# Kernel optimization log

Hardware: AMD Instinct MI355X
Metric: run time of the kernel (lower is better)

Reference implementation:

```python
import jax, jax.numpy as jnp
import numpy as np

R, N, B, S = 20, 4096, 16, 256          # relations, total nodes, graphs, nodes per graph
DIN, HID, H = 512, 128, 4               # in_dim, hidden_dim, num_heads
D = HID * H                              # flattened node-feature width (=512)
E = 16384                                # edges per relation
NEG_SLOPE = 0.2


def _gat(h, src, dst, W, al, ar, b):
    # DGL GATConv, eval mode (dropout off), identity residual (in == H*out), allow_zero_in_degree
    z = (h @ W).reshape(N, H, HID)                        # [N,H,Dh]
    el = (z * al).sum(-1)                                 # [N,H]
    er = (z * ar).sum(-1)                                 # [N,H]
    e = jax.nn.leaky_relu(el[src] + er[dst], NEG_SLOPE)   # [E,H]
    m = jax.ops.segment_max(e, dst, num_segments=N)       # per-dst max (edge softmax)
    ex = jnp.exp(e - m[dst])
    den = jax.ops.segment_sum(ex, dst, num_segments=N)
    alpha = ex / den[dst]                                 # [E,H]
    agg = jax.ops.segment_sum(alpha[..., None] * z[src], dst, num_segments=N)
    return agg + h.reshape(N, H, HID) + b, alpha


def _rgat_conv(h, src, dst, W, al, ar, b):
    # HeteroGraphConv with aggregate='mean' over R relations; scan keeps memory flat
    def body(acc, xs):
        s, d, Wr, alr, arr, br = xs
        out, alpha = _gat(h, s, d, Wr, alr, arr, br)
        return acc + out, alpha.mean(-1)                  # attention meaned over heads -> [E]
    acc, attn = jax.lax.scan(body, jnp.zeros((N, H, HID), h.dtype), (src, dst, W, al, ar, b))
    return acc / R, attn                                  # [N,H,Dh], [R,E]


def setup_inputs() -> dict:
    key = jax.random.key(0)
    ks = jax.random.split(key, 24)
    f32 = jnp.float32
    p = lambda k, shape: jax.random.normal(k, shape, f32) * 0.05
    z = lambda shape: jnp.zeros(shape, f32)
    return {
        'feat': jax.random.normal(ks[0], (N, DIN), f32),
        'hyp_emb': jax.random.normal(ks[1], (B, D), f32),
        'edge_src': jax.random.randint(ks[2], (R, E), 0, N),
        'edge_dst': jax.random.randint(ks[3], (R, E), 0, N),
        'W1': p(ks[4], (R, DIN, H * HID)), 'al1': p(ks[5], (R, H, HID)), 'ar1': p(ks[6], (R, H, HID)), 'b1': z((R, H, HID)),
        'W2': p(ks[7], (R, D, H * HID)), 'al2': p(ks[8], (R, H, HID)), 'ar2': p(ks[9], (R, H, HID)), 'b2': z((R, H, HID)),
        'Wq': p(ks[10], (D, D)), 'bq': z(D), 'Wk': p(ks[11], (D, D)), 'bk': z(D),
        'Wv': p(ks[12], (D, D)), 'bv': z(D), 'Wo': p(ks[13], (D, D)), 'bo': z(D),
        'Wn1': p(ks[14], (2 * D, HID)), 'bn1': z(HID), 'Wn2': p(ks[15], (HID, 2)), 'bn2': z(2),
    }


def reference(feat, hyp_emb, edge_src, edge_dst,
              W1, al1, ar1, b1, W2, al2, ar2, b2,
              Wq, bq, Wk, bk, Wv, bv, Wo, bo, Wn1, bn1, Wn2, bn2):
    # --- RGAT (rgat_generation) layer 1 + attention weights ---
    h1, attn = _rgat_conv(feat, edge_src, edge_dst, W1, al1, ar1, b1)
    h1 = jax.nn.elu(h1.reshape(N, D))
    # --- layer 2 ---
    h2, _ = _rgat_conv(h1, edge_src, edge_dst, W2, al2, ar2, b2)
    feats = h2.reshape(N, D)
    # --- node importance: scatter-add edge attention onto dst nodes, summed over etypes ---
    imp = jax.ops.segment_sum(attn.reshape(-1), edge_dst.reshape(-1), num_segments=N)
    feats_p = feats.reshape(B, S, D)                      # uniform graphs: split+pad == reshape
    weighted = feats_p * imp.reshape(B, S)[..., None]
    # --- MultiheadAttention(embed=D, heads=4): query = hyp_emb broadcast to all S positions ---
    Hm, Dm = 4, D // 4
    q = (hyp_emb @ Wq + bq).reshape(B, Hm, 1, Dm)         # identical query at every position
    k = (feats_p @ Wk + bk).reshape(B, S, Hm, Dm).transpose(0, 2, 1, 3)
    v = (feats_p @ Wv + bv).reshape(B, S, Hm, Dm).transpose(0, 2, 1, 3)
    scores = jnp.einsum('bhqd,bhkd->bhqk', q, k) / jnp.sqrt(jnp.float32(Dm))
    a = jax.nn.softmax(scores, axis=-1)                   # [B,Hm,1,S]
    ctx = jnp.einsum('bhqk,bhkd->bhqd', a, v).reshape(B, 1, D)
    attn_out = jnp.broadcast_to(ctx @ Wo + bo, (B, S, D))
    # --- node classifier on concat(weighted feats, attention output) ---
    combined = jnp.concatenate([weighted, attn_out], axis=-1).reshape(N, 2 * D)
    node_logits = jax.nn.relu(combined @ Wn1 + bn1) @ Wn2 + bn2
    return node_logits, attn
```

## Files before the change

### kernel.cpp

```cpp
#include <hip/hip_runtime.h>
#include <hip/hip_bf16.h>
#include <math.h>

#define NREL 20
#define NN   4096
#define NE   16384
#define DF   512
#define NHD  4
#define DHH  128
#define NB   16
#define NS   256

typedef __attribute__((ext_vector_type(8))) __bf16 bf16x8;
typedef __attribute__((ext_vector_type(4))) float f32x4;

__device__ inline float bf2f(unsigned short u) {
    union { float f; unsigned int i; } c; c.i = ((unsigned int)u) << 16; return c.f;
}
__device__ inline unsigned short f2bu(float f) {
    union { __hip_bfloat16 b; unsigned short u; } c; c.b = __float2bfloat16(f); return c.u;
}
__device__ inline void storeOut(float* p, float v) { *p = v; }
__device__ inline void storeOut(__hip_bfloat16* p, float v) { *p = __float2bfloat16(v); }

__device__ inline void load_lds16(const __hip_bfloat16* g, __hip_bfloat16* l) {
    __builtin_amdgcn_global_load_lds(
        (const __attribute__((address_space(1))) unsigned int*)(const void*)g,
        (__attribute__((address_space(3))) unsigned int*)(void*)l, 16, 0, 0);
}

__global__ void count_kernel(const int* __restrict__ dst, int* __restrict__ cnt) {
    int idx = blockIdx.x * 256 + threadIdx.x;
    int r = idx / NE;
    atomicAdd(&cnt[r * NN + dst[idx]], 1);
}

__global__ void sumcnt_kernel(const int* __restrict__ cnt, int* __restrict__ cntAll) {
    int n = blockIdx.x * 256 + threadIdx.x;
    int s = 0;
    #pragma unroll
    for (int r = 0; r < NREL; ++r) s += cnt[r * NN + n];
    cntAll[n] = s;
}

__global__ void scan_kernel(const int* __restrict__ cnt, int* __restrict__ rowptr,
                            int* __restrict__ woff) {
    int r = blockIdx.x;
    int t = threadIdx.x;
    __shared__ int sums[1024];
    int v[4]; int local = 0;
    #pragma unroll
    for (int j = 0; j < 4; ++j) { v[j] = cnt[r * NN + t * 4 + j]; local += v[j]; }
    sums[t] = local;
    __syncthreads();
    for (int off = 1; off < 1024; off <<= 1) {
        int x = (t >= off) ? sums[t - off] : 0;
        __syncthreads();
        sums[t] += x;
        __syncthreads();
    }
    int run = (t == 0) ? 0 : sums[t - 1];
    #pragma unroll
    for (int j = 0; j < 4; ++j) {
        rowptr[r * (NN + 1) + t * 4 + j] = run;
        woff[r * NN + t * 4 + j] = run;
        run += v[j];
    }
    if (t == 1023) rowptr[r * (NN + 1) + NN] = run;
}

__global__ void fill_kernel(const int* __restrict__ dst, const int* __restrict__ src,
                            int* __restrict__ woff, int* __restrict__ srcCSR,
                            int* __restrict__ eidCSR) {
    int idx = blockIdx.x * 256 + threadIdx.x;
    int r = idx / NE; int e = idx % NE;
    int pos = atomicAdd(&woff[r * NN + dst[idx]], 1);
    srcCSR[r * NE + pos] = src[idx];
    eidCSR[r * NE + pos] = e;
}

__global__ void cast_kernel(const float* __restrict__ in, unsigned short* __restrict__ out) {
    int i = blockIdx.x * 256 + threadIdx.x;
    float4 v = ((const float4*)in)[i];
    ushort4 o;
    o.x = f2bu(v.x); o.y = f2bu(v.y); o.z = f2bu(v.z); o.w = f2bu(v.w);
    ((ushort4*)out)[i] = o;
}

__global__ void biassum_kernel(const float* __restrict__ bmat, float* __restrict__ bsum) {
    int f = blockIdx.x * 256 + threadIdx.x;
    float s = 0.f;
    #pragma unroll
    for (int r = 0; r < NREL; ++r) s += bmat[r * DF + f];
    bsum[f] = s;
}

__global__ __launch_bounds__(256) void transw_kernel(
    const float* __restrict__ W, __hip_bfloat16* __restrict__ Wt, int K, int N)
{
    int r = blockIdx.z;
    __shared__ float t[32][33];
    int k0 = blockIdx.x * 32, n0 = blockIdx.y * 32;
    int tx = threadIdx.x % 32, ty = threadIdx.x / 32;
    #pragma unroll
    for (int kk = ty; kk < 32; kk += 8)
        t[kk][tx] = W[((size_t)r * K + k0 + kk) * N + n0 + tx];
    __syncthreads();
    #pragma unroll
    for (int nn = ty; nn < 32; nn += 8)
        Wt[((size_t)r * N + n0 + nn) * K + k0 + tx] = __float2bfloat16(t[tx][nn]);
}

template <typename OutT, bool RELU, bool FUSE>
__global__ __launch_bounds__(256) void mfma_gemm(
    const __hip_bfloat16* __restrict__ A,
    const __hip_bfloat16* __restrict__ BtAll,
    const float* __restrict__ bias,
    OutT* __restrict__ Call, int M, int N, int K,
    const float* __restrict__ al, const float* __restrict__ ar,
    float* __restrict__ el, float* __restrict__ er)
{
    int r = blockIdx.z;
    const __hip_bfloat16* Bt = BtAll + (size_t)r * N * K;
    OutT* C = Call + (size_t)r * M * N;
    const int rowBase = blockIdx.y * 128;
    const int colBase = blockIdx.x * 128;
    __shared__ __hip_bfloat16 As[128 * 32];
    __shared__ __hip_bfloat16 Bs[128 * 32];
    const int tid = threadIdx.x;
    const int w = tid >> 6, l = tid & 63;
    const int wr = w >> 1, wc = w & 1;
    const int m15 = l & 15, q = l >> 4;
    const int sRow = w * 16 + (l >> 2);
    const int sKs = (((l & 3) ^ ((l >> 3) & 3))) * 8;
    const __hip_bfloat16* Ag0 = A + (size_t)(rowBase + sRow) * K + sKs;
    const __hip_bfloat16* Ag1 = Ag0 + (size_t)64 * K;
    const __hip_bfloat16* Bg0 = Bt + (size_t)(colBase + sRow) * K + sKs;
    const __hip_bfloat16* Bg1 = Bg0 + (size_t)64 * K;
    __hip_bfloat16* Asl0 = As + sRow * 32 + (l & 3) * 8;
    __hip_bfloat16* Asl1 = Asl0 + 2048;
    __hip_bfloat16* Bsl0 = Bs + sRow * 32 + (l & 3) * 8;
    __hip_bfloat16* Bsl1 = Bsl0 + 2048;
    const int swf = (m15 >> 1) & 3;

    f32x4 acc[4][4];
    #pragma unroll
    for (int i = 0; i < 4; ++i)
        #pragma unroll
        for (int j = 0; j < 4; ++j) acc[i][j] = (f32x4){0.f, 0.f, 0.f, 0.f};

    for (int k0 = 0; k0 < K; k0 += 32) {
        load_lds16(Ag0 + k0, Asl0);
        load_lds16(Ag1 + k0, Asl1);
        load_lds16(Bg0 + k0, Bsl0);
        load_lds16(Bg1 + k0, Bsl1);
        __syncthreads();
        bf16x8 a[4], b[4];
        #pragma unroll
        for (int i = 0; i < 4; ++i)
            a[i] = *(const bf16x8*)&As[(wr * 64 + i * 16 + m15) * 32 + (q ^ swf) * 8];
        #pragma unroll
        for (int j = 0; j < 4; ++j)
            b[j] = *(const bf16x8*)&Bs[(wc * 64 + j * 16 + m15) * 32 + (q ^ swf) * 8];
        #pragma unroll
        for (int i = 0; i < 4; ++i)
            #pragma unroll
            for (int j = 0; j < 4; ++j)
                acc[i][j] = __builtin_amdgcn_mfma_f32_16x16x32_bf16(a[i], b[j], acc[i][j], 0, 0, 0);
        __syncthreads();
    }

    #pragma unroll
    for (int i = 0; i < 4; ++i) {
        #pragma unroll
        for (int j = 0; j < 4; ++j) {
            int col = colBase + wc * 64 + j * 16 + m15;
            float bv = bias ? bias[col] : 0.f;
            #pragma unroll
            for (int reg = 0; reg < 4; ++reg) {
                int row = rowBase + wr * 64 + i * 16 + q * 4 + reg;
                float v = acc[i][j][reg] + bv;
                if (RELU) v = fmaxf(v, 0.f);
                storeOut(&C[(size_t)row * N + col], v);
            }
        }
    }

    if (FUSE) {
        float alv[4], arv[4];
        #pragma unroll
        for (int j = 0; j < 4; ++j) {
            int col = colBase + wc * 64 + j * 16 + m15;
            alv[j] = al[r * DF + col];
            arv[j] = ar[r * DF + col];
        }
        float pe[4][4], pr[4][4];
        #pragma unroll
        for (int i = 0; i < 4; ++i)
            #pragma unroll
            for (int reg = 0; reg < 4; ++reg) {
                float se = 0.f, sr = 0.f;
                #pragma unroll
                for (int j = 0; j < 4; ++j) {
                    se += acc[i][j][reg] * alv[j];
                    sr += acc[i][j][reg] * arv[j];
                }
                pe[i][reg] = se; pr[i][reg] = sr;
            }
        #pragma unroll
        for (int off = 1; off < 16; off <<= 1)
            #pragma unroll
            for (int i = 0; i < 4; ++i)
                #pragma unroll
                for (int reg = 0; reg < 4; ++reg) {
                    pe[i][reg] += __shfl_xor(pe[i][reg], off);
                    pr[i][reg] += __shfl_xor(pr[i][reg], off);
                }
        float* eP = (float*)As;
        float* rP = eP + 256;
        if (m15 == 0) {
            #pragma unroll
            for (int i = 0; i < 4; ++i)
                #pragma unroll
                for (int reg = 0; reg < 4; ++reg) {
                    int rowL = wr * 64 + i * 16 + q * 4 + reg;
                    eP[rowL * 2 + wc] = pe[i][reg];
                    rP[rowL * 2 + wc] = pr[i][reg];
                }
        }
        __syncthreads();
        if (tid < 128) {
            int head = colBase >> 7;
            size_t idx = ((size_t)r * NN + rowBase + tid) * NHD + head;
            el[idx] = eP[tid * 2] + eP[tid * 2 + 1];
            er[idx] = rP[tid * 2] + rP[tid * 2 + 1];
        }
    }
}

template <typename OutT>
__global__ __launch_bounds__(256) void gemm_kernel(
    const float* __restrict__ A, const float* __restrict__ Bm,
    const float* __restrict__ bias, OutT* __restrict__ C,
    int M, int K, int Nn)
{
    int r = blockIdx.z;
    const float* B = Bm + (size_t)r * K * Nn;
    OutT* Cr = C + (size_t)r * M * Nn;
    int rowBase = blockIdx.y * 64;
    int colBase = blockIdx.x * 64;
    __shared__ float As[64][17];
    __shared__ float Bs[16][64];
    int tid = threadIdx.x;
    int tx = tid % 16, ty = tid / 16;
    float acc[4][4] = {};
    int aRow = tid / 4, aK4 = (tid % 4) * 4;
    int bK = tid / 16, bN4 = (tid % 16) * 4;
    for (int k0 = 0; k0 < K; k0 += 16) {
        int gRow = rowBase + aRow;
        float4 av = make_float4(0.f, 0.f, 0.f, 0.f);
        if (gRow < M) av = *(const float4*)(A + (size_t)gRow * K + k0 + aK4);
        As[aRow][aK4 + 0] = av.x; As[aRow][aK4 + 1] = av.y;
        As[aRow][aK4 + 2] = av.z; As[aRow][aK4 + 3] = av.w;
        float4 bv = *(const float4*)(B + (size_t)(k0 + bK) * Nn + colBase + bN4);
        *(float4*)&Bs[bK][bN4] = bv;
        __syncthreads();
        #pragma unroll
        for (int k = 0; k < 16; ++k) {
            float a[4], b[4];
            #pragma unroll
            for (int i = 0; i < 4; ++i) a[i] = As[ty * 4 + i][k];
            #pragma unroll
            for (int j = 0; j < 4; ++j) b[j] = Bs[k][tx * 4 + j];
            #pragma unroll
            for (int i = 0; i < 4; ++i)
                #pragma unroll
                for (int j = 0; j < 4; ++j) acc[i][j] += a[i] * b[j];
        }
        __syncthreads();
    }
    #pragma unroll
    for (int i = 0; i < 4; ++i) {
        int gRow = rowBase + ty * 4 + i;
        if (gRow >= M) continue;
        #pragma unroll
        for (int j = 0; j < 4; ++j) {
            int gCol = colBase + tx * 4 + j;
            float v = acc[i][j];
            if (bias) v += bias[gCol];
            storeOut(&Cr[(size_t)gRow * Nn + gCol], v);
        }
    }
}

__global__ __launch_bounds__(256) void alpha_kernel(
    const float* __restrict__ el, const float* __restrict__ er,
    const int* __restrict__ rowptr, const int* __restrict__ rowptr2,
    const int* __restrict__ cnt, const int* __restrict__ srcCSR,
    const int* __restrict__ eidCSR,
    float* __restrict__ alphaPk, int* __restrict__ srcPk,
    float* __restrict__ attn, float* __restrict__ imp)
{
    int t = blockIdx.x * 256 + threadIdx.x;
    int r = t / NN, n = t % NN;
    int start = rowptr[r * (NN + 1) + n];
    int d = rowptr[r * (NN + 1) + n + 1] - start;
    if (d == 0) return;
    float4 er4 = *(const float4*)&er[((size_t)r * NN + n) * NHD];
    float4 den = make_float4(0.f, 0.f, 0.f, 0.f);
    for (int j = 0; j < d; ++j) {
        int s = srcCSR[r * NE + start + j];
        float4 el4 = *(const float4*)&el[((size_t)r * NN + s) * NHD];
        float v0 = el4.x + er4.x; v0 = v0 > 0.f ? v0 : 0.2f * v0;
        float v1 = el4.y + er4.y; v1 = v1 > 0.f ? v1 : 0.2f * v1;
        float v2 = el4.z + er4.z; v2 = v2 > 0.f ? v2 : 0.2f * v2;
        float v3 = el4.w + er4.w; v3 = v3 > 0.f ? v3 : 0.2f * v3;
        den.x += __expf(v0); den.y += __expf(v1);
        den.z += __expf(v2); den.w += __expf(v3);
    }
    float4 inv = make_float4(1.f / den.x, 1.f / den.y, 1.f / den.z, 1.f / den.w);
    int pbase = rowptr2[n];
    for (int rp = 0; rp < r; ++rp) pbase += cnt[rp * NN + n];
    float impLoc = 0.f;
    for (int j = 0; j < d; ++j) {
        int s = srcCSR[r * NE + start + j];
        float4 el4 = *(const float4*)&el[((size_t)r * NN + s) * NHD];
        float v0 = el4.x + er4.x; v0 = v0 > 0.f ? v0 : 0.2f * v0;
        float v1 = el4.y + er4.y; v1 = v1 > 0.f ? v1 : 0.2f * v1;
        float v2 = el4.z + er4.z; v2 = v2 > 0.f ? v2 : 0.2f * v2;
        float v3 = el4.w + er4.w; v3 = v3 > 0.f ? v3 : 0.2f * v3;
        float4 a4 = make_float4(__expf(v0) * inv.x, __expf(v1) * inv.y,
                                __expf(v2) * inv.z, __expf(v3) * inv.w);
        *(float4*)&alphaPk[(size_t)(pbase + j) * 4] = a4;
        srcPk[pbase + j] = r * NN + s;
        if (attn) {
            float a = 0.25f * (a4.x + a4.y + a4.z + a4.w);
            attn[r * NE + eidCSR[r * NE + start + j]] = a;
            impLoc += a;
        }
    }
    if (attn) atomicAdd(&imp[n], impLoc);
}

__global__ __launch_bounds__(256) void aggc_kernel(
    const __hip_bfloat16* __restrict__ Z,
    const int* __restrict__ rowptr2, const int* __restrict__ srcPk,
    const float* __restrict__ alphaPk, const float* __restrict__ bsum,
    const float* __restrict__ hin, float* __restrict__ hout,
    __hip_bfloat16* __restrict__ hout_bf, int applyElu)
{
    int n = blockIdx.x;
    int w = threadIdx.x >> 6, lane = threadIdx.x & 63;
    int h = lane >> 4;
    int base = rowptr2[n];
    int deg = rowptr2[n + 1] - base;
    float acc[8] = {};
    int i = w * 2;
    int z0 = 0, z1 = 0; float a0 = 0.f, a1 = 0.f;
    if (i < deg)     { z0 = srcPk[base + i];     a0 = alphaPk[(size_t)(base + i) * 4 + h]; }
    if (i + 1 < deg) { z1 = srcPk[base + i + 1]; a1 = alphaPk[(size_t)(base + i + 1) * 4 + h]; }
    while (i < deg) {
        int cz0 = z0, cz1 = z1; float ca0 = a0, ca1 = a1;
        int ni = i + 8;
        if (ni < deg)     { z0 = srcPk[base + ni];     a0 = alphaPk[(size_t)(base + ni) * 4 + h]; }
        if (ni + 1 < deg) { z1 = srcPk[base + ni + 1]; a1 = alphaPk[(size_t)(base + ni + 1) * 4 + h]; }
        else a1 = 0.f;
        float4 r0 = *(const float4*)&Z[(size_t)cz0 * DF + lane * 8];
        float4 r1 = *(const float4*)&Z[(size_t)cz1 * DF + lane * 8];
        const unsigned short* u0 = (const unsigned short*)&r0;
        const unsigned short* u1 = (const unsigned short*)&r1;
        #pragma unroll
        for (int j = 0; j < 8; ++j) acc[j] += ca0 * bf2f(u0[j]) + ca1 * bf2f(u1[j]);
        i = ni;
    }
    __shared__ float red[4][DF];
    #pragma unroll
    for (int j = 0; j < 8; ++j) red[w][lane * 8 + j] = acc[j];
    __syncthreads();
    const float invR = 1.0f / NREL;
    int f = threadIdx.x;
    #pragma unroll
    for (int rep = 0; rep < 2; ++rep, f += 256) {
        float v = red[0][f] + red[1][f] + red[2][f] + red[3][f];
        v = (v + bsum[f]) * invR + hin[(size_t)n * DF + f];
        if (applyElu) v = v > 0.f ? v : expm1f(v);
        hout[(size_t)n * DF + f] = v;
        hout_bf[(size_t)n * DF + f] = __float2bfloat16(v);
    }
}

__global__ __launch_bounds__(256) void mha_scores(
    const float* __restrict__ q, const float* __restrict__ k,
    float* __restrict__ scores)
{
    int b = blockIdx.x;
    int w = threadIdx.x >> 6, lane = threadIdx.x & 63;
    int s = blockIdx.y * 4 + w;
    const float4* qp = (const float4*)&q[(size_t)b * DF + lane * 8];
    const float4* kp = (const float4*)&k[((size_t)(b * NS + s)) * DF + lane * 8];
    float4 q0 = qp[0], q1 = qp[1];
    float4 k0 = kp[0], k1 = kp[1];
    float p = q0.x * k0.x + q0.y * k0.y + q0.z * k0.z + q0.w * k0.w
            + q1.x * k1.x + q1.y * k1.y + q1.z * k1.z + q1.w * k1.w;
    #pragma unroll
    for (int off = 1; off < 16; off <<= 1) p += __shfl_xor(p, off);
    if ((lane & 15) == 0) {
        int h = lane >> 4;
        scores[((size_t)(b * NHD + h)) * NS + s] = p * 0.08838834764831845f;
    }
}

__global__ __launch_bounds__(256) void mha_soft(float* __restrict__ scores) {
    int b = blockIdx.x;
    int h = threadIdx.x >> 6, lane = threadIdx.x & 63;
    float* sp = &scores[((size_t)(b * NHD + h)) * NS];
    float v[4];
    float mx = -INFINITY;
    #pragma unroll
    for (int i = 0; i < 4; ++i) { v[i] = sp[lane + 64 * i]; mx = fmaxf(mx, v[i]); }
    #pragma unroll
    for (int off = 32; off; off >>= 1) mx = fmaxf(mx, __shfl_xor(mx, off));
    float sum = 0.f;
    #pragma unroll
    for (int i = 0; i < 4; ++i) { v[i] = __expf(v[i] - mx); sum += v[i]; }
    #pragma unroll
    for (int off = 32; off; off >>= 1) sum += __shfl_xor(sum, off);
    float inv = 1.0f / sum;
    #pragma unroll
    for (int i = 0; i < 4; ++i) sp[lane + 64 * i] = v[i] * inv;
}

__global__ __launch_bounds__(256) void mha_ctx(
    const float* __restrict__ scores, const float* __restrict__ v,
    float* __restrict__ ctx)
{
    int b = blockIdx.x, h = blockIdx.y;
    int t = threadIdx.x;
    int d = t & 127, half = t >> 7;
    __shared__ float a_s[NS];
    a_s[t] = scores[((size_t)(b * NHD + h)) * NS + t];
    __syncthreads();
    float acc = 0.f;
    const float* vp = &v[((size_t)(b * NS + half * 128)) * DF + h * DHH + d];
    #pragma unroll 4
    for (int i = 0; i < 128; ++i)
        acc += a_s[half * 128 + i] * vp[(size_t)i * DF];
    __shared__ float red[256];
    red[t] = acc;
    __syncthreads();
    if (t < 128) ctx[(size_t)b * DF + h * DHH + t] = red[t] + red[t + 128];
}

__global__ __launch_bounds__(256) void combined_kernel(
    const float* __restrict__ feats, const float* __restrict__ imp,
    const float* __restrict__ abuf, __hip_bfloat16* __restrict__ comb)
{
    int n = blockIdx.x;
    int t = threadIdx.x;
    int b = n >> 8;
    float im = imp[n];
    #pragma unroll
    for (int rep = 0; rep < 4; ++rep) {
        int f = t + rep * 256;
        float v = (f < DF) ? feats[(size_t)n * DF + f] * im
                           : abuf[(size_t)b * DF + (f - DF)];
        comb[(size_t)n * (2 * DF) + f] = __float2bfloat16(v);
    }
}

__global__ __launch_bounds__(256) void cls2_kernel(
    const float* __restrict__ hidden, const float* __restrict__ Wn2,
    const float* __restrict__ bn2, float* __restrict__ out)
{
    __shared__ float w2[256];
    int t = threadIdx.x;
    w2[t] = Wn2[t];
    __syncthreads();
    int n = blockIdx.x * 256 + t;
    const float* hp = &hidden[(size_t)n * 128];
    float p0 = bn2[0], p1 = bn2[1];
    #pragma unroll 4
    for (int kk = 0; kk < 128; ++kk) {
        float hv = hp[kk];
        p0 += hv * w2[kk * 2 + 0];
        p1 += hv * w2[kk * 2 + 1];
    }
    out[n * 2 + 0] = p0;
    out[n * 2 + 1] = p1;
}

extern "C" void kernel_launch(void* const* d_in, const int* in_sizes, int n_in,
                              void* d_out, int out_size, void* d_ws, size_t ws_size,
                              hipStream_t stream) {
    const float* feat = (const float*)d_in[0];
    const float* hyp  = (const float*)d_in[1];
    const int*   esrc = (const int*)d_in[2];
    const int*   edst = (const int*)d_in[3];
    const float* W1   = (const float*)d_in[4];
    const float* al1  = (const float*)d_in[5];
    const float* ar1  = (const float*)d_in[6];
    const float* b1   = (const float*)d_in[7];
    const float* W2   = (const float*)d_in[8];
    const float* al2  = (const float*)d_in[9];
    const float* ar2  = (const float*)d_in[10];
    const float* b2   = (const float*)d_in[11];
    const float* Wq = (const float*)d_in[12]; const float* bq = (const float*)d_in[13];
    const float* Wk = (const float*)d_in[14]; const float* bk = (const float*)d_in[15];
    const float* Wv = (const float*)d_in[16]; const float* bv = (const float*)d_in[17];
    const float* Wo = (const float*)d_in[18]; const float* bo = (const float*)d_in[19];
    const float* Wn1 = (const float*)d_in[20]; const float* bn1 = (const float*)d_in[21];
    const float* Wn2 = (const float*)d_in[22]; const float* bn2 = (const float*)d_in[23];

    char* ws = (char*)d_ws;
    size_t off = 0;
    auto alloc = [&](size_t bytes) -> void* {
        void* p = ws + off;
        off += (bytes + 255) & ~(size_t)255;
        return p;
    };
    __hip_bfloat16* Z = (__hip_bfloat16*)alloc((size_t)NREL * NN * DF * 2);
    float* el     = (float*)alloc((size_t)NREL * NN * NHD * 4);
    float* er     = (float*)alloc((size_t)NREL * NN * NHD * 4);
    int* rowptr   = (int*)alloc((size_t)NREL * (NN + 1) * 4);
    int* rowptr2  = (int*)alloc((size_t)(NN + 1) * 4);
    int* woff     = (int*)alloc((size_t)NREL * NN * 4);
    int* woff2    = (int*)alloc((size_t)NN * 4);
    int* srcCSR   = (int*)alloc((size_t)NREL * NE * 4);
    int* eidCSR   = (int*)alloc((size_t)NREL * NE * 4);
    int* cnt      = (int*)alloc((size_t)NREL * NN * 4);
    int* cntAll   = (int*)alloc((size_t)NN * 4);
    int* srcPk    = (int*)alloc((size_t)NREL * NE * 4);
    float* alphaPk= (float*)alloc((size_t)NREL * NE * NHD * 4);
    float* bsum   = (float*)alloc((size_t)DF * 4);
    float* h1     = (float*)alloc((size_t)NN * DF * 4);
    float* feats  = (float*)alloc((size_t)NN * DF * 4);
    float* imp    = (float*)alloc((size_t)NN * 4);
    float* kbuf   = (float*)alloc((size_t)NN * DF * 4);
    float* vbuf   = (float*)alloc((size_t)NN * DF * 4);
    float* qbuf   = (float*)alloc((size_t)NB * DF * 4);
    float* ctxb   = (float*)alloc((size_t)NB * DF * 4);
    float* abuf   = (float*)alloc((size_t)NB * DF * 4);
    float* scoresb= (float*)alloc((size_t)NB * NHD * NS * 4);
    float* hidden = (float*)alloc((size_t)NN * 128 * 4);
    __hip_bfloat16* featbf  = (__hip_bfloat16*)alloc((size_t)NN * DF * 2);
    __hip_bfloat16* h1bf    = (__hip_bfloat16*)alloc((size_t)NN * DF * 2);
    __hip_bfloat16* featsbf = (__hip_bfloat16*)alloc((size_t)NN * DF * 2);
    __hip_bfloat16* combbf  = (__hip_bfloat16*)alloc((size_t)NN * 2 * DF * 2);
    __hip_bfloat16* Wt1 = (__hip_bfloat16*)alloc((size_t)NREL * DF * DF * 2);
    __hip_bfloat16* Wt2 = (__hip_bfloat16*)alloc((size_t)NREL * DF * DF * 2);
    __hip_bfloat16* WtK = (__hip_bfloat16*)alloc((size_t)DF * DF * 2);
    __hip_bfloat16* WtV = (__hip_bfloat16*)alloc((size_t)DF * DF * 2);
    __hip_bfloat16* Wn1t = (__hip_bfloat16*)alloc((size_t)(2 * DF) * 128 * 2);
    if (off > ws_size) return;

    float* logits = (float*)d_out;
    float* attn   = (float*)d_out + (size_t)NN * 2;

    hipMemsetAsync(cnt, 0, (size_t)NREL * NN * 4, stream);
    hipMemsetAsync(imp, 0, (size_t)NN * 4, stream);
    count_kernel<<<NREL * NE / 256, 256, 0, stream>>>(edst, cnt);
    sumcnt_kernel<<<NN / 256, 256, 0, stream>>>(cnt, cntAll);
    scan_kernel<<<NREL, 1024, 0, stream>>>(cnt, rowptr, woff);
    scan_kernel<<<1, 1024, 0, stream>>>(cntAll, rowptr2, woff2);
    fill_kernel<<<NREL * NE / 256, 256, 0, stream>>>(edst, esrc, woff, srcCSR, eidCSR);

    cast_kernel<<<NN * DF / 1024, 256, 0, stream>>>(feat, (unsigned short*)featbf);
    transw_kernel<<<dim3(DF / 32, DF / 32, NREL), 256, 0, stream>>>(W1, Wt1, DF, DF);
    transw_kernel<<<dim3(DF / 32, DF / 32, NREL), 256, 0, stream>>>(W2, Wt2, DF, DF);
    transw_kernel<<<dim3(DF / 32, DF / 32, 1), 256, 0, stream>>>(Wk, WtK, DF, DF);
    transw_kernel<<<dim3(DF / 32, DF / 32, 1), 256, 0, stream>>>(Wv, WtV, DF, DF);
    transw_kernel<<<dim3(2 * DF / 32, 128 / 32, 1), 256, 0, stream>>>(Wn1, Wn1t, 2 * DF, 128);

    mfma_gemm<__hip_bfloat16, false, true><<<dim3(DF / 128, NN / 128, NREL), 256, 0, stream>>>(
        featbf, Wt1, nullptr, Z, NN, DF, DF, al1, ar1, el, er);
    biassum_kernel<<<DF / 256, 256, 0, stream>>>(b1, bsum);
    alpha_kernel<<<NREL * NN / 256, 256, 0, stream>>>(
        el, er, rowptr, rowptr2, cnt, srcCSR, eidCSR, alphaPk, srcPk, attn, imp);
    aggc_kernel<<<NN, 256, 0, stream>>>(Z, rowptr2, srcPk, alphaPk, bsum,
                                        feat, h1, h1bf, 1);

    mfma_gemm<__hip_bfloat16, false, true><<<dim3(DF / 128, NN / 128, NREL), 256, 0, stream>>>(
        h1bf, Wt2, nullptr, Z, NN, DF, DF, al2, ar2, el, er);
    biassum_kernel<<<DF / 256, 256, 0, stream>>>(b2, bsum);
    alpha_kernel<<<NREL * NN / 256, 256, 0, stream>>>(
        el, er, rowptr, rowptr2, cnt, srcCSR, eidCSR, alphaPk, srcPk, nullptr, nullptr);
    aggc_kernel<<<NN, 256, 0, stream>>>(Z, rowptr2, srcPk, alphaPk, bsum,
                                        h1, feats, featsbf, 0);

    mfma_gemm<float, false, false><<<dim3(DF / 128, NN / 128, 1), 256, 0, stream>>>(
        featsbf, WtK, bk, kbuf, NN, DF, DF, nullptr, nullptr, nullptr, nullptr);
    mfma_gemm<float, false, false><<<dim3(DF / 128, NN / 128, 1), 256, 0, stream>>>(
        featsbf, WtV, bv, vbuf, NN, DF, DF, nullptr, nullptr, nullptr, nullptr);
    gemm_kernel<float><<<dim3(DF / 64, 1, 1), 256, 0, stream>>>(
        hyp, Wq, bq, qbuf, NB, DF, DF);
    mha_scores<<<dim3(NB, NS / 4), 256, 0, stream>>>(qbuf, kbuf, scoresb);
    mha_soft<<<NB, 256, 0, stream>>>(scoresb);
    mha_ctx<<<dim3(NB, NHD), 256, 0, stream>>>(scoresb, vbuf, ctxb);
    gemm_kernel<float><<<dim3(DF / 64, 1, 1), 256, 0, stream>>>(
        ctxb, Wo, bo, abuf, NB, DF, DF);

    combined_kernel<<<NN, 256, 0, stream>>>(feats, imp, abuf, combbf);
    mfma_gemm<float, true, false><<<dim3(1, NN / 128, 1), 256, 0, stream>>>(
        combbf, Wn1t, bn1, hidden, NN, 128, 2 * DF, nullptr, nullptr, nullptr, nullptr);
    cls2_kernel<<<NN / 256, 256, 0, stream>>>(hidden, Wn2, bn2, logits);
}
```

Baseline: 666.1 us.

## Merge prep and scan launches, batch K/V GEMMs, pre-swizzle GEMM operands

Folds the feature cast, the bias sums, the buffer zeroing and the K/V bias packing into one prep kernel. The global-count scan is merged into the per-relation scan launch, and the K and V projections run as a single batched GEMM. The LDS bank-conflict XOR swizzle moves out of the GEMM's global address and into the producer kernels, which now write operands already swizzled. This cuts launch count and per-load index math, but every producer must now match the swizzle layout exactly.

```diff
diff --git a/kernel.cpp b/kernel.cpp
--- a/kernel.cpp
+++ b/kernel.cpp
@@ -29,28 +29,72 @@
         (__attribute__((address_space(3))) unsigned int*)(void*)l, 16, 0, 0);
 }
 
+__device__ inline int kswz(int f, int row) { return f ^ ((((row) >> 1) & 3) << 3); }
+
+__global__ __launch_bounds__(256) void prep_kernel(
+    const float* __restrict__ feat, unsigned short* __restrict__ featbf,
+    const float* __restrict__ b1, const float* __restrict__ b2,
+    const float* __restrict__ bk, const float* __restrict__ bv,
+    float* __restrict__ bsum1, float* __restrict__ bsum2,
+    float* __restrict__ bkv, int* __restrict__ cnt, float* __restrict__ imp)
+{
+    int blk = blockIdx.x, t = threadIdx.x;
+    if (blk < 1024) {
+        int idx = blk * 256 + t;
+        int row = idx >> 6;
+        int f = (idx & 63) * 8;
+        int fs = kswz(f, row);
+        const float4* ip = (const float4*)&feat[(size_t)row * DF + f];
+        float4 v0 = ip[0], v1 = ip[1];
+        union { unsigned short u[8]; uint4 q; } o;
+        o.u[0] = f2bu(v0.x); o.u[1] = f2bu(v0.y); o.u[2] = f2bu(v0.z); o.u[3] = f2bu(v0.w);
+        o.u[4] = f2bu(v1.x); o.u[5] = f2bu(v1.y); o.u[6] = f2bu(v1.z); o.u[7] = f2bu(v1.w);
+        *(uint4*)(featbf + (size_t)row * DF + fs) = o.q;
+    } else if (blk == 1024) {
+        #pragma unroll
+        for (int rep = 0; rep < 2; ++rep) {
+            int f = t + rep * 256;
+            float s1 = 0.f, s2 = 0.f;
+            #pragma unroll
+            for (int r = 0; r < NREL; ++r) { s1 += b1[r * DF + f]; s2 += b2[r * DF + f]; }
+            bsum1[f] = s1; bsum2[f] = s2;
+        }
+        for (int i = t; i < NN; i += 256) imp[i] = 0.f;
+    } else if (blk == 1025) {
+        #pragma unroll
+        for (int j = 0; j < 4; ++j) {
+            int f = t + j * 256;
+            bkv[f] = (f < DF) ? bk[f] : bv[f - DF];
+        }
+    } else {
+        int idx = (blk - 1026) * 256 + t;
+        cnt[idx] = 0;
+    }
+}
+
 __global__ void count_kernel(const int* __restrict__ dst, int* __restrict__ cnt) {
     int idx = blockIdx.x * 256 + threadIdx.x;
     int r = idx / NE;
     atomicAdd(&cnt[r * NN + dst[idx]], 1);
 }
 
-__global__ void sumcnt_kernel(const int* __restrict__ cnt, int* __restrict__ cntAll) {
-    int n = blockIdx.x * 256 + threadIdx.x;
-    int s = 0;
-    #pragma unroll
-    for (int r = 0; r < NREL; ++r) s += cnt[r * NN + n];
-    cntAll[n] = s;
-}
-
 __global__ void scan_kernel(const int* __restrict__ cnt, int* __restrict__ rowptr,
-                            int* __restrict__ woff) {
+                            int* __restrict__ woff, int* __restrict__ rowptr2) {
     int r = blockIdx.x;
     int t = threadIdx.x;
     __shared__ int sums[1024];
     int v[4]; int local = 0;
-    #pragma unroll
-    for (int j = 0; j < 4; ++j) { v[j] = cnt[r * NN + t * 4 + j]; local += v[j]; }
+    if (r < NREL) {
+        #pragma unroll
+        for (int j = 0; j < 4; ++j) { v[j] = cnt[r * NN + t * 4 + j]; local += v[j]; }
+    } else {
+        #pragma unroll
+        for (int j = 0; j < 4; ++j) {
+            int s = 0;
+            for (int rel = 0; rel < NREL; ++rel) s += cnt[rel * NN + t * 4 + j];
+            v[j] = s; local += s;
+        }
+    }
     sums[t] = local;
     __syncthreads();
     for (int off = 1; off < 1024; off <<= 1) {
@@ -60,13 +104,19 @@
         __syncthreads();
     }
     int run = (t == 0) ? 0 : sums[t - 1];
-    #pragma unroll
-    for (int j = 0; j < 4; ++j) {
-        rowptr[r * (NN + 1) + t * 4 + j] = run;
-        woff[r * NN + t * 4 + j] = run;
-        run += v[j];
-    }
-    if (t == 1023) rowptr[r * (NN + 1) + NN] = run;
+    if (r < NREL) {
+        #pragma unroll
+        for (int j = 0; j < 4; ++j) {
+            rowptr[r * (NN + 1) + t * 4 + j] = run;
+            woff[r * NN + t * 4 + j] = run;
+            run += v[j];
+        }
+        if (t == 1023) rowptr[r * (NN + 1) + NN] = run;
+    } else {
+        #pragma unroll
+        for (int j = 0; j < 4; ++j) { rowptr2[t * 4 + j] = run; run += v[j]; }
+        if (t == 1023) rowptr2[NN] = run;
+    }
 }
 
 __global__ void fill_kernel(const int* __restrict__ dst, const int* __restrict__ src,
@@ -79,22 +129,6 @@
     eidCSR[r * NE + pos] = e;
 }
 
-__global__ void cast_kernel(const float* __restrict__ in, unsigned short* __restrict__ out) {
-    int i = blockIdx.x * 256 + threadIdx.x;
-    float4 v = ((const float4*)in)[i];
-    ushort4 o;
-    o.x = f2bu(v.x); o.y = f2bu(v.y); o.z = f2bu(v.z); o.w = f2bu(v.w);
-    ((ushort4*)out)[i] = o;
-}
-
-__global__ void biassum_kernel(const float* __restrict__ bmat, float* __restrict__ bsum) {
-    int f = blockIdx.x * 256 + threadIdx.x;
-    float s = 0.f;
-    #pragma unroll
-    for (int r = 0; r < NREL; ++r) s += bmat[r * DF + f];
-    bsum[f] = s;
-}
-
 __global__ __launch_bounds__(256) void transw_kernel(
     const float* __restrict__ W, __hip_bfloat16* __restrict__ Wt, int K, int N)
 {
@@ -107,15 +141,37 @@
         t[kk][tx] = W[((size_t)r * K + k0 + kk) * N + n0 + tx];
     __syncthreads();
     #pragma unroll
-    for (int nn = ty; nn < 32; nn += 8)
-        Wt[((size_t)r * N + n0 + nn) * K + k0 + tx] = __float2bfloat16(t[tx][nn]);
+    for (int nn = ty; nn < 32; nn += 8) {
+        int row = n0 + nn;
+        Wt[((size_t)r * N + row) * K + k0 + kswz(tx, row)] = __float2bfloat16(t[tx][nn]);
+    }
+}
+
+__global__ __launch_bounds__(256) void transw_kv_kernel(
+    const float* __restrict__ Wk, const float* __restrict__ Wv,
+    __hip_bfloat16* __restrict__ Wt)
+{
+    int z = blockIdx.z;
+    const float* W = z ? Wv : Wk;
+    __shared__ float t[32][33];
+    int k0 = blockIdx.x * 32, n0 = blockIdx.y * 32;
+    int tx = threadIdx.x % 32, ty = threadIdx.x / 32;
+    #pragma unroll
+    for (int kk = ty; kk < 32; kk += 8)
+        t[kk][tx] = W[(size_t)(k0 + kk) * DF + n0 + tx];
+    __syncthreads();
+    #pragma unroll
+    for (int nn = ty; nn < 32; nn += 8) {
+        int row = n0 + nn;
+        Wt[((size_t)z * DF + row) * DF + k0 + kswz(tx, row)] = __float2bfloat16(t[tx][nn]);
+    }
 }
 
 template <typename OutT, bool RELU, bool FUSE>
 __global__ __launch_bounds__(256) void mfma_gemm(
     const __hip_bfloat16* __restrict__ A,
     const __hip_bfloat16* __restrict__ BtAll,
-    const float* __restrict__ bias,
+    const float* __restrict__ bias, int biasStride,
     OutT* __restrict__ Call, int M, int N, int K,
     const float* __restrict__ al, const float* __restrict__ ar,
     float* __restrict__ el, float* __restrict__ er)
@@ -132,14 +188,14 @@
     const int wr = w >> 1, wc = w & 1;
     const int m15 = l & 15, q = l >> 4;
     const int sRow = w * 16 + (l >> 2);
-    const int sKs = (((l & 3) ^ ((l >> 3) & 3))) * 8;
-    const __hip_bfloat16* Ag0 = A + (size_t)(rowBase + sRow) * K + sKs;
+    const int sK = (l & 3) * 8;
+    const __hip_bfloat16* Ag0 = A + (size_t)(rowBase + sRow) * K + sK;
     const __hip_bfloat16* Ag1 = Ag0 + (size_t)64 * K;
-    const __hip_bfloat16* Bg0 = Bt + (size_t)(colBase + sRow) * K + sKs;
+    const __hip_bfloat16* Bg0 = Bt + (size_t)(colBase + sRow) * K + sK;
     const __hip_bfloat16* Bg1 = Bg0 + (size_t)64 * K;
-    __hip_bfloat16* Asl0 = As + sRow * 32 + (l & 3) * 8;
+    __hip_bfloat16* Asl0 = As + sRow * 32 + sK;
     __hip_bfloat16* Asl1 = Asl0 + 2048;
-    __hip_bfloat16* Bsl0 = Bs + sRow * 32 + (l & 3) * 8;
+    __hip_bfloat16* Bsl0 = Bs + sRow * 32 + sK;
     __hip_bfloat16* Bsl1 = Bsl0 + 2048;
     const int swf = (m15 >> 1) & 3;
 
@@ -175,7 +231,7 @@
         #pragma unroll
         for (int j = 0; j < 4; ++j) {
             int col = colBase + wc * 64 + j * 16 + m15;
-            float bv = bias ? bias[col] : 0.f;
+            float bv = bias ? bias[r * biasStride + col] : 0.f;
             #pragma unroll
             for (int reg = 0; reg < 4; ++reg) {
                 int row = rowBase + wr * 64 + i * 16 + q * 4 + reg;
@@ -378,6 +434,7 @@
     for (int j = 0; j < 8; ++j) red[w][lane * 8 + j] = acc[j];
     __syncthreads();
     const float invR = 1.0f / NREL;
+    const int sw = ((n >> 1) & 3) << 3;
     int f = threadIdx.x;
     #pragma unroll
     for (int rep = 0; rep < 2; ++rep, f += 256) {
@@ -385,7 +442,7 @@
         v = (v + bsum[f]) * invR + hin[(size_t)n * DF + f];
         if (applyElu) v = v > 0.f ? v : expm1f(v);
         hout[(size_t)n * DF + f] = v;
-        hout_bf[(size_t)n * DF + f] = __float2bfloat16(v);
+        hout_bf[(size_t)n * DF + (f ^ sw)] = __float2bfloat16(v);
     }
 }
 
@@ -459,12 +516,13 @@
     int t = threadIdx.x;
     int b = n >> 8;
     float im = imp[n];
+    const int sw = ((n >> 1) & 3) << 3;
     #pragma unroll
     for (int rep = 0; rep < 4; ++rep) {
         int f = t + rep * 256;
         float v = (f < DF) ? feats[(size_t)n * DF + f] * im
                            : abuf[(size_t)b * DF + (f - DF)];
-        comb[(size_t)n * (2 * DF) + f] = __float2bfloat16(v);
+        comb[(size_t)n * (2 * DF) + (f ^ sw)] = __float2bfloat16(v);
     }
 }
 
@@ -524,19 +582,18 @@
     int* rowptr   = (int*)alloc((size_t)NREL * (NN + 1) * 4);
     int* rowptr2  = (int*)alloc((size_t)(NN + 1) * 4);
     int* woff     = (int*)alloc((size_t)NREL * NN * 4);
-    int* woff2    = (int*)alloc((size_t)NN * 4);
     int* srcCSR   = (int*)alloc((size_t)NREL * NE * 4);
     int* eidCSR   = (int*)alloc((size_t)NREL * NE * 4);
     int* cnt      = (int*)alloc((size_t)NREL * NN * 4);
-    int* cntAll   = (int*)alloc((size_t)NN * 4);
     int* srcPk    = (int*)alloc((size_t)NREL * NE * 4);
     float* alphaPk= (float*)alloc((size_t)NREL * NE * NHD * 4);
-    float* bsum   = (float*)alloc((size_t)DF * 4);
+    float* bsum1  = (float*)alloc((size_t)DF * 4);
+    float* bsum2  = (float*)alloc((size_t)DF * 4);
+    float* bkv    = (float*)alloc((size_t)2 * DF * 4);
     float* h1     = (float*)alloc((size_t)NN * DF * 4);
     float* feats  = (float*)alloc((size_t)NN * DF * 4);
     float* imp    = (float*)alloc((size_t)NN * 4);
-    float* kbuf   = (float*)alloc((size_t)NN * DF * 4);
-    float* vbuf   = (float*)alloc((size_t)NN * DF * 4);
+    float* kvbuf  = (float*)alloc((size_t)2 * NN * DF * 4);
     float* qbuf   = (float*)alloc((size_t)NB * DF * 4);
     float* ctxb   = (float*)alloc((size_t)NB * DF * 4);
     float* abuf   = (float*)alloc((size_t)NB * DF * 4);
@@ -548,49 +605,43 @@
     __hip_bfloat16* combbf  = (__hip_bfloat16*)alloc((size_t)NN * 2 * DF * 2);
     __hip_bfloat16* Wt1 = (__hip_bfloat16*)alloc((size_t)NREL * DF * DF * 2);
     __hip_bfloat16* Wt2 = (__hip_bfloat16*)alloc((size_t)NREL * DF * DF * 2);
-    __hip_bfloat16* WtK = (__hip_bfloat16*)alloc((size_t)DF * DF * 2);
-    __hip_bfloat16* WtV = (__hip_bfloat16*)alloc((size_t)DF * DF * 2);
+    __hip_bfloat16* WtKV = (__hip_bfloat16*)alloc((size_t)2 * DF * DF * 2);
     __hip_bfloat16* Wn1t = (__hip_bfloat16*)alloc((size_t)(2 * DF) * 128 * 2);
     if (off > ws_size) return;
 
     float* logits = (float*)d_out;
     float* attn   = (float*)d_out + (size_t)NN * 2;
-
-    hipMemsetAsync(cnt, 0, (size_t)NREL * NN * 4, stream);
-    hipMemsetAsync(imp, 0, (size_t)NN * 4, stream);
+    float* kbuf = kvbuf;
+    float* vbuf = kvbuf + (size_t)NN * DF;
+
+    prep_kernel<<<1026 + NREL * NN / 256, 256, 0, stream>>>(
+        feat, (unsigned short*)featbf, b1, b2, bk, bv, bsum1, bsum2, bkv, cnt, imp);
+
     count_kernel<<<NREL * NE / 256, 256, 0, stream>>>(edst, cnt);
-    sumcnt_kernel<<<NN / 256, 256, 0, stream>>>(cnt, cntAll);
-    scan_kernel<<<NREL, 1024, 0, stream>>>(cnt, rowptr, woff);
-    scan_kernel<<<1, 1024, 0, stream>>>(cntAll, rowptr2, woff2);
+    scan_kernel<<<NREL + 1, 1024, 0, stream>>>(cnt, rowptr, woff, rowptr2);
     fill_kernel<<<NREL * NE / 256, 256, 0, stream>>>(edst, esrc, woff, srcCSR, eidCSR);
 
-    cast_kernel<<<NN * DF / 1024, 256, 0, stream>>>(feat, (unsigned short*)featbf);
     transw_kernel<<<dim3(DF / 32, DF / 32, NREL), 256, 0, stream>>>(W1, Wt1, DF, DF);
     transw_kernel<<<dim3(DF / 32, DF / 32, NREL), 256, 0, stream>>>(W2, Wt2, DF, DF);
-    transw_kernel<<<dim3(DF / 32, DF / 32, 1), 256, 0, stream>>>(Wk, WtK, DF, DF);
-    transw_kernel<<<dim3(DF / 32, DF / 32, 1), 256, 0, stream>>>(Wv, WtV, DF, DF);
+    transw_kv_kernel<<<dim3(DF / 32, DF / 32, 2), 256, 0, stream>>>(Wk, Wv, WtKV);
     transw_kernel<<<dim3(2 * DF / 32, 128 / 32, 1), 256, 0, stream>>>(Wn1, Wn1t, 2 * DF, 128);
 
     mfma_gemm<__hip_bfloat16, false, true><<<dim3(DF / 128, NN / 128, NREL), 256, 0, stream>>>(
-        featbf, Wt1, nullptr, Z, NN, DF, DF, al1, ar1, el, er);
-    biassum_kernel<<<DF / 256, 256, 0, stream>>>(b1, bsum);
+        featbf, Wt1, nullptr, 0, Z, NN, DF, DF, al1, ar1, el, er);
     alpha_kernel<<<NREL * NN / 256, 256, 0, stream>>>(
         el, er, rowptr, rowptr2, cnt, srcCSR, eidCSR, alphaPk, srcPk, attn, imp);
-    aggc_kernel<<<NN, 256, 0, stream>>>(Z, rowptr2, srcPk, alphaPk, bsum,
+    aggc_kernel<<<NN, 256, 0, stream>>>(Z, rowptr2, srcPk, alphaPk, bsum1,
                                         feat, h1, h1bf, 1);
 
     mfma_gemm<__hip_bfloat16, false, true><<<dim3(DF / 128, NN / 128, NREL), 256, 0, stream>>>(
-        h1bf, Wt2, nullptr, Z, NN, DF, DF, al2, ar2, el, er);
-    biassum_kernel<<<DF / 256, 256, 0, stream>>>(b2, bsum);
+        h1bf, Wt2, nullptr, 0, Z, NN, DF, DF, al2, ar2, el, er);
     alpha_kernel<<<NREL * NN / 256, 256, 0, stream>>>(
         el, er, rowptr, rowptr2, cnt, srcCSR, eidCSR, alphaPk, srcPk, nullptr, nullptr);
-    aggc_kernel<<<NN, 256, 0, stream>>>(Z, rowptr2, srcPk, alphaPk, bsum,
+    aggc_kernel<<<NN, 256, 0, stream>>>(Z, rowptr2, srcPk, alphaPk, bsum2,
                                         h1, feats, featsbf, 0);
 
-    mfma_gemm<float, false, false><<<dim3(DF / 128, NN / 128, 1), 256, 0, stream>>>(
-        featsbf, WtK, bk, kbuf, NN, DF, DF, nullptr, nullptr, nullptr, nullptr);
-    mfma_gemm<float, false, false><<<dim3(DF / 128, NN / 128, 1), 256, 0, stream>>>(
-        featsbf, WtV, bv, vbuf, NN, DF, DF, nullptr, nullptr, nullptr, nullptr);
+    mfma_gemm<float, false, false><<<dim3(DF / 128, NN / 128, 2), 256, 0, stream>>>(
+        featsbf, WtKV, bkv, DF, kvbuf, NN, DF, DF, nullptr, nullptr, nullptr, nullptr);
     gemm_kernel<float><<<dim3(DF / 64, 1, 1), 256, 0, stream>>>(
         hyp, Wq, bq, qbuf, NB, DF, DF);
     mha_scores<<<dim3(NB, NS / 4), 256, 0, stream>>>(qbuf, kbuf, scoresb);
@@ -601,6 +652,6 @@
 
     combined_kernel<<<NN, 256, 0, stream>>>(feats, imp, abuf, combbf);
     mfma_gemm<float, true, false><<<dim3(1, NN / 128, 1), 256, 0, stream>>>(
-        combbf, Wn1t, bn1, hidden, NN, 128, 2 * DF, nullptr, nullptr, nullptr, nullptr);
+        combbf, Wn1t, bn1, 0, hidden, NN, 128, 2 * DF, nullptr, nullptr, nullptr, nullptr);
     cls2_kernel<<<NN / 256, 256, 0, stream>>>(hidden, Wn2, bn2, logits);
 }
```

Result: faster. 641.2 us (-3.7%).
